# Kernel tuning notes

Measured on AMD Instinct MI355X. Metric: run time of the kernel, lower is better.

## Reference

```python
import jax, jax.numpy as jnp
import numpy as np

HIDDEN = 256


def setup_inputs() -> dict:
    key = jax.random.key(0)
    ks = jax.random.split(key, 6)
    b, c_len, q_len, h = 32, 1024, 128, HIDDEN
    # Xavier-uniform bounds for the learned weights
    lim_vec = float(np.sqrt(6.0 / (h + 1)))      # (h, 1) weights
    lim_cq = float(np.sqrt(6.0 / (1 + h)))       # (1, 1, h) weight
    return {
        "context": jax.random.normal(ks[0], (b, c_len, h), dtype=jnp.float32),
        "query": jax.random.normal(ks[1], (b, q_len, h), dtype=jnp.float32),
        "c_mask": jnp.zeros((b, c_len), dtype=bool),
        "q_mask": jnp.zeros((b, q_len), dtype=bool),
        "c_weight": jax.random.uniform(ks[2], (h, 1), jnp.float32, -lim_vec, lim_vec),
        "q_weight": jax.random.uniform(ks[3], (h, 1), jnp.float32, -lim_vec, lim_vec),
        "cq_weight": jax.random.uniform(ks[4], (1, 1, h), jnp.float32, -lim_cq, lim_cq),
        "bias": jnp.zeros((1,), dtype=jnp.float32),
    }


def reference(context, query, c_mask, q_mask, c_weight, q_weight, cq_weight, bias):
    # Trilinear similarity: S[b,i,j] = c_i.w_c + q_j.w_q + (c_i * w_cq).q_j + bias
    s0 = context @ c_weight                                  # (b, c, 1)
    s1 = jnp.swapaxes(query @ q_weight, 1, 2)                # (b, 1, q)
    s2 = jnp.einsum('bch,bqh->bcq', context * cq_weight, query)
    S = s0 + s1 + s2 + bias                                  # (b, c, q)

    S_bar = jax.nn.softmax(S, axis=1)       # softmax over context axis
    S_bar_bar = jax.nn.softmax(S, axis=2)   # softmax over query axis

    A = jnp.einsum('bcq,bqh->bch', S, query)  # note: raw S, as in source
    B = jnp.einsum('bcq,bkq,bkh->bch', S_bar, S_bar_bar, context)

    return jnp.concatenate([context, A, context * A, context * B], axis=2)
```

## Files before the change

### kernel.cpp

```cpp
#include <hip/hip_runtime.h>
#include <cstdint>
#include <cstddef>

#define BATCH 32
#define CLEN  1024
#define QLEN  128
#define HID   256

typedef __attribute__((ext_vector_type(8))) short bf16x8;
typedef __attribute__((ext_vector_type(4))) float f32x4;

#define MFMA(a, b, c) __builtin_amdgcn_mfma_f32_16x16x32_bf16((a), (b), (c), 0, 0, 0)

__device__ __forceinline__ ushort f2b(float f) {
    union { float f; uint u; } v; v.f = f;
    uint r = (v.u + 0x7fffu + ((v.u >> 16) & 1u)) >> 16;
    return (ushort)r;
}
__device__ __forceinline__ float b2f(ushort u) {
    union { uint u; float f; } v; v.u = ((uint)u) << 16;
    return v.f;
}

__global__ __launch_bounds__(256) void prep_kernel(
    const float* __restrict__ context, const float* __restrict__ query,
    const float* __restrict__ cw, const float* __restrict__ qw,
    const float* __restrict__ cqw,
    ushort* __restrict__ ctxT, ushort* __restrict__ mcB,
    ushort* __restrict__ qB, ushort* __restrict__ qT,
    float* __restrict__ cdot, float* __restrict__ qdot)
{
    __shared__ ushort lds[64][258];
    int bid = blockIdx.x;
    int t = threadIdx.x;
    int r = t >> 2, qd = t & 3;
    if (bid < 512) {
        int b = bid >> 4, c0 = (bid & 15) * 64;
        const float* src = context + ((size_t)(b * CLEN + c0 + r)) * HID;
        ushort* mcr = mcB + ((size_t)(b * CLEN + c0 + r)) * HID;
        float dot = 0.f;
        #pragma unroll
        for (int j = 0; j < 16; j++) {
            int h = j * 16 + qd * 4;
            float4 v  = *reinterpret_cast<const float4*>(src + h);
            float4 w  = *reinterpret_cast<const float4*>(cw + h);
            float4 wc = *reinterpret_cast<const float4*>(cqw + h);
            dot += v.x * w.x + v.y * w.y + v.z * w.z + v.w * w.w;
            uint p0 = (uint)f2b(v.x) | ((uint)f2b(v.y) << 16);
            uint p1 = (uint)f2b(v.z) | ((uint)f2b(v.w) << 16);
            *reinterpret_cast<uint*>(&lds[r][h])     = p0;
            *reinterpret_cast<uint*>(&lds[r][h + 2]) = p1;
            uint2 mc;
            mc.x = (uint)f2b(v.x * wc.x) | ((uint)f2b(v.y * wc.y) << 16);
            mc.y = (uint)f2b(v.z * wc.z) | ((uint)f2b(v.w * wc.w) << 16);
            *reinterpret_cast<uint2*>(mcr + h) = mc;
        }
        dot += __shfl_xor(dot, 1);
        dot += __shfl_xor(dot, 2);
        if (qd == 0) cdot[b * CLEN + c0 + r] = dot;
        __syncthreads();
        ushort* dst = ctxT + ((size_t)(b * HID + t)) * CLEN + c0;
        #pragma unroll
        for (int j = 0; j < 8; j++) {
            uint4 w;
            w.x = (uint)lds[j*8+0][t] | ((uint)lds[j*8+1][t] << 16);
            w.y = (uint)lds[j*8+2][t] | ((uint)lds[j*8+3][t] << 16);
            w.z = (uint)lds[j*8+4][t] | ((uint)lds[j*8+5][t] << 16);
            w.w = (uint)lds[j*8+6][t] | ((uint)lds[j*8+7][t] << 16);
            *reinterpret_cast<uint4*>(dst + j * 8) = w;
        }
    } else {
        int bb = bid - 512;
        int b = bb >> 1, q0 = (bb & 1) * 64;
        const float* src = query + ((size_t)(b * QLEN + q0 + r)) * HID;
        ushort* qBr = qB + ((size_t)(b * QLEN + q0 + r)) * HID;
        float dot = 0.f;
        #pragma unroll
        for (int j = 0; j < 16; j++) {
            int h = j * 16 + qd * 4;
            float4 v = *reinterpret_cast<const float4*>(src + h);
            float4 w = *reinterpret_cast<const float4*>(qw + h);
            dot += v.x * w.x + v.y * w.y + v.z * w.z + v.w * w.w;
            uint p0 = (uint)f2b(v.x) | ((uint)f2b(v.y) << 16);
            uint p1 = (uint)f2b(v.z) | ((uint)f2b(v.w) << 16);
            *reinterpret_cast<uint*>(&lds[r][h])     = p0;
            *reinterpret_cast<uint*>(&lds[r][h + 2]) = p1;
            uint2 pk; pk.x = p0; pk.y = p1;
            *reinterpret_cast<uint2*>(qBr + h) = pk;
        }
        dot += __shfl_xor(dot, 1);
        dot += __shfl_xor(dot, 2);
        if (qd == 0) qdot[b * QLEN + q0 + r] = dot;
        __syncthreads();
        ushort* dst = qT + ((size_t)(b * HID + t)) * QLEN + q0;
        #pragma unroll
        for (int j = 0; j < 8; j++) {
            uint4 w;
            w.x = (uint)lds[j*8+0][t] | ((uint)lds[j*8+1][t] << 16);
            w.y = (uint)lds[j*8+2][t] | ((uint)lds[j*8+3][t] << 16);
            w.z = (uint)lds[j*8+4][t] | ((uint)lds[j*8+5][t] << 16);
            w.w = (uint)lds[j*8+6][t] | ((uint)lds[j*8+7][t] << 16);
            *reinterpret_cast<uint4*>(dst + j * 8) = w;
        }
    }
}

__global__ __launch_bounds__(256) void s_kernel(
    const ushort* __restrict__ mcB, const ushort* __restrict__ qB,
    const float* __restrict__ cdot, const float* __restrict__ qdot,
    const float* __restrict__ bias,
    ushort* __restrict__ S, ushort* __restrict__ P2T)
{
    __shared__ float ldsS[64][132];
    __shared__ float ldsM[64], ldsR[64];
    int ct = blockIdx.x, b = blockIdx.y;
    int c0 = ct * 64;
    int t = threadIdx.x;
    int w = t >> 6, L = t & 63, g = L >> 4, ln = L & 15;
    int wr = w >> 1, wc = w & 1;

    f32x4 acc[2][4];
    #pragma unroll
    for (int mi = 0; mi < 2; mi++)
        #pragma unroll
        for (int ni = 0; ni < 4; ni++) acc[mi][ni] = (f32x4){0.f, 0.f, 0.f, 0.f};

    const ushort* aBase = mcB + ((size_t)(b * CLEN + c0 + wr * 32)) * HID;
    const ushort* qBb   = qB + ((size_t)(b * QLEN + wc * 64)) * HID;

    #pragma unroll 2
    for (int kk = 0; kk < 8; kk++) {
        int k = kk * 32 + g * 8;
        bf16x8 a[2], bq[4];
        #pragma unroll
        for (int mi = 0; mi < 2; mi++)
            a[mi] = *reinterpret_cast<const bf16x8*>(aBase + (size_t)(mi * 16 + ln) * HID + k);
        #pragma unroll
        for (int ni = 0; ni < 4; ni++)
            bq[ni] = *reinterpret_cast<const bf16x8*>(qBb + (size_t)(ni * 16 + ln) * HID + k);
        #pragma unroll
        for (int mi = 0; mi < 2; mi++)
            #pragma unroll
            for (int ni = 0; ni < 4; ni++)
                acc[mi][ni] = MFMA(a[mi], bq[ni], acc[mi][ni]);
    }

    float bv = bias[0];
    float qdv[4];
    #pragma unroll
    for (int ni = 0; ni < 4; ni++) qdv[ni] = qdot[b * QLEN + wc * 64 + ni * 16 + ln];
    #pragma unroll
    for (int mi = 0; mi < 2; mi++)
        #pragma unroll
        for (int r = 0; r < 4; r++) {
            int row = wr * 32 + mi * 16 + g * 4 + r;
            float cd = cdot[b * CLEN + c0 + row] + bv;
            #pragma unroll
            for (int ni = 0; ni < 4; ni++)
                ldsS[row][wc * 64 + ni * 16 + ln] = acc[mi][ni][r] + cd + qdv[ni];
        }
    __syncthreads();
    {
        int row = t >> 2, qs = (t & 3) * 32;
        float4 vr[8];
        float m = -1e30f;
        #pragma unroll
        for (int j = 0; j < 8; j++) {
            vr[j] = *reinterpret_cast<const float4*>(&ldsS[row][qs + j * 4]);
            m = fmaxf(m, fmaxf(fmaxf(vr[j].x, vr[j].y), fmaxf(vr[j].z, vr[j].w)));
        }
        m = fmaxf(m, __shfl_xor(m, 1));
        m = fmaxf(m, __shfl_xor(m, 2));
        float s = 0.f;
        #pragma unroll
        for (int j = 0; j < 8; j++)
            s += __expf(vr[j].x - m) + __expf(vr[j].y - m) +
                 __expf(vr[j].z - m) + __expf(vr[j].w - m);
        s += __shfl_xor(s, 1);
        s += __shfl_xor(s, 2);
        if ((t & 3) == 0) { ldsM[row] = m; ldsR[row] = 1.0f / s; }
    }
    __syncthreads();
    {
        const size_t Sbase = ((size_t)b * CLEN + c0) * QLEN;
        #pragma unroll
        for (int i = 0; i < 8; i++) {
            int flat = t + 256 * i;
            int q4 = flat & 31, c = flat >> 5;
            float4 v = *reinterpret_cast<const float4*>(&ldsS[c][q4 * 4]);
            uint2 pk;
            pk.x = (uint)f2b(v.x) | ((uint)f2b(v.y) << 16);
            pk.y = (uint)f2b(v.z) | ((uint)f2b(v.w) << 16);
            *reinterpret_cast<uint2*>(&S[Sbase + (size_t)c * QLEN + q4 * 4]) = pk;
        }
    }
    {
        int q = t >> 1, half = t & 1;
        ushort* dst = P2T + ((size_t)b * QLEN + q) * CLEN + c0 + half * 32;
        #pragma unroll
        for (int jo = 0; jo < 4; jo++) {
            uint pk[4];
            #pragma unroll
            for (int l = 0; l < 4; l++) {
                int c0l = half * 32 + jo * 8 + l * 2;
                float p0 = __expf(ldsS[c0l][q]     - ldsM[c0l])     * ldsR[c0l];
                float p1 = __expf(ldsS[c0l + 1][q] - ldsM[c0l + 1]) * ldsR[c0l + 1];
                pk[l] = (uint)f2b(p0) | ((uint)f2b(p1) << 16);
            }
            uint4 wv; wv.x = pk[0]; wv.y = pk[1]; wv.z = pk[2]; wv.w = pk[3];
            *reinterpret_cast<uint4*>(dst + jo * 8) = wv;
        }
    }
}

__global__ __launch_bounds__(256) void t_kernel(
    const ushort* __restrict__ ctxT, const ushort* __restrict__ P2T,
    float* __restrict__ Tpart)
{
    int x = blockIdx.x, b = blockIdx.y;
    int h0 = (x >> 1) * 64, ks = x & 1;
    int t = threadIdx.x;
    int w = t >> 6, L = t & 63, g = L >> 4, ln = L & 15;
    int wr = w >> 1, wc = w & 1;

    f32x4 acc[2][4];
    #pragma unroll
    for (int mi = 0; mi < 2; mi++)
        #pragma unroll
        for (int ni = 0; ni < 4; ni++) acc[mi][ni] = (f32x4){0.f, 0.f, 0.f, 0.f};

    const ushort* aB = ctxT + ((size_t)(b * HID + h0 + wr * 32)) * CLEN + ks * 512;
    const ushort* bB = P2T + ((size_t)(b * QLEN + wc * 64)) * CLEN + ks * 512;

    #pragma unroll 2
    for (int kk = 0; kk < 16; kk++) {
        int k = kk * 32 + g * 8;
        bf16x8 a[2], bq[4];
        #pragma unroll
        for (int mi = 0; mi < 2; mi++)
            a[mi] = *reinterpret_cast<const bf16x8*>(aB + (size_t)(mi * 16 + ln) * CLEN + k);
        #pragma unroll
        for (int ni = 0; ni < 4; ni++)
            bq[ni] = *reinterpret_cast<const bf16x8*>(bB + (size_t)(ni * 16 + ln) * CLEN + k);
        #pragma unroll
        for (int mi = 0; mi < 2; mi++)
            #pragma unroll
            for (int ni = 0; ni < 4; ni++)
                acc[mi][ni] = MFMA(a[mi], bq[ni], acc[mi][ni]);
    }
    float* dst = Tpart + (size_t)ks * (BATCH * HID * QLEN);
    #pragma unroll
    for (int mi = 0; mi < 2; mi++)
        #pragma unroll
        for (int ni = 0; ni < 4; ni++)
            #pragma unroll
            for (int r = 0; r < 4; r++) {
                int h = h0 + wr * 32 + mi * 16 + g * 4 + r;
                int q = wc * 64 + ni * 16 + ln;
                dst[((size_t)b * HID + h) * QLEN + q] = acc[mi][ni][r];
            }
}

__global__ __launch_bounds__(256) void ct_kernel(
    const ushort* __restrict__ S, const float* __restrict__ Tpart,
    ushort* __restrict__ Tt, float* __restrict__ colmax)
{
    __shared__ float red[4][2][8];
    __shared__ float MS[16], SR[16];
    int qc = blockIdx.x, b = blockIdx.y;
    int q0 = qc * 16;
    int t = threadIdx.x;
    int qh = t & 1, cg = t >> 1;
    int w = t >> 6, L = t & 63;
    const ushort* base = S + (size_t)b * CLEN * QLEN + q0 + qh * 8;
    float vm[8];
    #pragma unroll
    for (int j = 0; j < 8; j++) vm[j] = -1e30f;
    #pragma unroll
    for (int i = 0; i < 8; i++) {
        bf16x8 v = *reinterpret_cast<const bf16x8*>(base + (size_t)(cg + 128 * i) * QLEN);
        #pragma unroll
        for (int j = 0; j < 8; j++) vm[j] = fmaxf(vm[j], b2f((ushort)v[j]));
    }
    #pragma unroll
    for (int off = 2; off <= 32; off <<= 1)
        #pragma unroll
        for (int j = 0; j < 8; j++) vm[j] = fmaxf(vm[j], __shfl_xor(vm[j], off, 64));
    if (L < 2) {
        #pragma unroll
        for (int j = 0; j < 8; j++) red[w][L][j] = vm[j];
    }
    __syncthreads();
    if (t < 16) {
        int j = t & 7, qq = t >> 3;
        float m = fmaxf(fmaxf(red[0][qq][j], red[1][qq][j]),
                        fmaxf(red[2][qq][j], red[3][qq][j]));
        MS[qq * 8 + j] = m;
        colmax[b * QLEN + q0 + qq * 8 + j] = m;
    }
    __syncthreads();
    float M[8], sum[8];
    #pragma unroll
    for (int j = 0; j < 8; j++) { M[j] = MS[qh * 8 + j]; sum[j] = 0.f; }
    #pragma unroll
    for (int i = 0; i < 8; i++) {
        bf16x8 v = *reinterpret_cast<const bf16x8*>(base + (size_t)(cg + 128 * i) * QLEN);
        #pragma unroll
        for (int j = 0; j < 8; j++) sum[j] += __expf(b2f((ushort)v[j]) - M[j]);
    }
    #pragma unroll
    for (int off = 2; off <= 32; off <<= 1)
        #pragma unroll
        for (int j = 0; j < 8; j++) sum[j] += __shfl_xor(sum[j], off, 64);
    __syncthreads();
    if (L < 2) {
        #pragma unroll
        for (int j = 0; j < 8; j++) red[w][L][j] = sum[j];
    }
    __syncthreads();
    if (t < 16) {
        int j = t & 7, qq = t >> 3;
        float s = red[0][qq][j] + red[1][qq][j] + red[2][qq][j] + red[3][qq][j];
        SR[qq * 8 + j] = 1.0f / s;
    }
    __syncthreads();
    const float* p0 = Tpart + ((size_t)b * HID + t) * QLEN + q0;
    const float* p1 = p0 + (size_t)BATCH * HID * QLEN;
    uint pk[8];
    #pragma unroll
    for (int seg = 0; seg < 4; seg++) {
        float4 xa = *reinterpret_cast<const float4*>(p0 + seg * 4);
        float4 xb = *reinterpret_cast<const float4*>(p1 + seg * 4);
        float r0 = (xa.x + xb.x) * SR[seg * 4 + 0];
        float r1 = (xa.y + xb.y) * SR[seg * 4 + 1];
        float r2 = (xa.z + xb.z) * SR[seg * 4 + 2];
        float r3 = (xa.w + xb.w) * SR[seg * 4 + 3];
        pk[seg * 2 + 0] = (uint)f2b(r0) | ((uint)f2b(r1) << 16);
        pk[seg * 2 + 1] = (uint)f2b(r2) | ((uint)f2b(r3) << 16);
    }
    ushort* dst = Tt + ((size_t)b * HID + t) * QLEN + q0;
    uint4 w0; w0.x = pk[0]; w0.y = pk[1]; w0.z = pk[2]; w0.w = pk[3];
    uint4 w1; w1.x = pk[4]; w1.y = pk[5]; w1.z = pk[6]; w1.w = pk[7];
    *reinterpret_cast<uint4*>(dst)     = w0;
    *reinterpret_cast<uint4*>(dst + 8) = w1;
}

__global__ __launch_bounds__(256) void ab_out_kernel(
    const ushort* __restrict__ S, const ushort* __restrict__ qT,
    const ushort* __restrict__ Tt, const float* __restrict__ context,
    const float* __restrict__ colmax, float* __restrict__ out)
{
    __shared__ float ldsA[64][68];
    __shared__ float ldsB[64][68];
    int x = blockIdx.x, b = blockIdx.y;
    int c0 = (x >> 1) * 64, h0 = (x & 1) * 128;
    int t = threadIdx.x;
    int wc = t >> 6, L = t & 63, g = L >> 4, ln = L & 15;

    f32x4 accA[4][2], accB[4][2];
    #pragma unroll
    for (int mi = 0; mi < 4; mi++)
        #pragma unroll
        for (int ni = 0; ni < 2; ni++) {
            accA[mi][ni] = (f32x4){0.f, 0.f, 0.f, 0.f};
            accB[mi][ni] = (f32x4){0.f, 0.f, 0.f, 0.f};
        }

    const ushort* Srow = S + ((size_t)(b * CLEN + c0)) * QLEN;
    const ushort* qTb  = qT + ((size_t)(b * HID + h0 + wc * 32)) * QLEN;
    const ushort* TtB  = Tt + ((size_t)(b * HID + h0 + wc * 32)) * QLEN;
    const float* cmB = colmax + b * QLEN;

    #pragma unroll
    for (int kk = 0; kk < 4; kk++) {
        int k = kk * 32 + g * 8;
        float4 cm0 = *reinterpret_cast<const float4*>(cmB + k);
        float4 cm1 = *reinterpret_cast<const float4*>(cmB + k + 4);
        float cmv[8] = {cm0.x, cm0.y, cm0.z, cm0.w, cm1.x, cm1.y, cm1.z, cm1.w};
        bf16x8 sa[4], pa[4], bq[2], bt[2];
        #pragma unroll
        for (int mi = 0; mi < 4; mi++) {
            sa[mi] = *reinterpret_cast<const bf16x8*>(Srow + (size_t)(mi * 16 + ln) * QLEN + k);
            bf16x8 pv;
            #pragma unroll
            for (int i = 0; i < 8; i++)
                pv[i] = (short)f2b(__expf(b2f((ushort)sa[mi][i]) - cmv[i]));
            pa[mi] = pv;
        }
        #pragma unroll
        for (int ni = 0; ni < 2; ni++) {
            bq[ni] = *reinterpret_cast<const bf16x8*>(qTb + (size_t)(ni * 16 + ln) * QLEN + k);
            bt[ni] = *reinterpret_cast<const bf16x8*>(TtB + (size_t)(ni * 16 + ln) * QLEN + k);
        }
        #pragma unroll
        for (int mi = 0; mi < 4; mi++)
            #pragma unroll
            for (int ni = 0; ni < 2; ni++) {
                accA[mi][ni] = MFMA(sa[mi], bq[ni], accA[mi][ni]);
                accB[mi][ni] = MFMA(pa[mi], bt[ni], accB[mi][ni]);
            }
    }

    #pragma unroll
    for (int hh = 0; hh < 2; hh++) {
        if ((wc >> 1) == hh) {
            int hc = wc & 1;
            #pragma unroll
            for (int mi = 0; mi < 4; mi++)
                #pragma unroll
                for (int ni = 0; ni < 2; ni++)
                    #pragma unroll
                    for (int r = 0; r < 4; r++) {
                        ldsA[mi * 16 + g * 4 + r][hc * 32 + ni * 16 + ln] = accA[mi][ni][r];
                        ldsB[mi * 16 + g * 4 + r][hc * 32 + ni * 16 + ln] = accB[mi][ni][r];
                    }
        }
        __syncthreads();
        #pragma unroll
        for (int i = 0; i < 4; i++) {
            int flat = t + 256 * i;
            int h4 = flat & 15, c = flat >> 4;
            float4 av = *reinterpret_cast<const float4*>(&ldsA[c][h4 * 4]);
            float4 bv = *reinterpret_cast<const float4*>(&ldsB[c][h4 * 4]);
            float4 cv = *reinterpret_cast<const float4*>(
                context + ((size_t)(b * CLEN + c0 + c)) * HID + h0 + hh * 64 + h4 * 4);
            size_t o = ((size_t)(b * CLEN + c0 + c)) * 1024 + h0 + hh * 64 + h4 * 4;
            *reinterpret_cast<float4*>(&out[o])       = cv;
            *reinterpret_cast<float4*>(&out[o + 256]) = av;
            *reinterpret_cast<float4*>(&out[o + 512]) =
                make_float4(cv.x * av.x, cv.y * av.y, cv.z * av.z, cv.w * av.w);
            *reinterpret_cast<float4*>(&out[o + 768]) =
                make_float4(cv.x * bv.x, cv.y * bv.y, cv.z * bv.z, cv.w * bv.w);
        }
        __syncthreads();
    }
}

extern "C" void kernel_launch(void* const* d_in, const int* in_sizes, int n_in,
                              void* d_out, int out_size, void* d_ws, size_t ws_size,
                              hipStream_t stream)
{
    (void)in_sizes; (void)n_in; (void)out_size; (void)ws_size;
    const float* context   = (const float*)d_in[0];
    const float* query     = (const float*)d_in[1];
    const float* c_weight  = (const float*)d_in[4];
    const float* q_weight  = (const float*)d_in[5];
    const float* cq_weight = (const float*)d_in[6];
    const float* bias      = (const float*)d_in[7];
    float* out = (float*)d_out;
    char* wsb  = (char*)d_ws;

    ushort* ctxT = (ushort*)(wsb);
    ushort* mcB  = (ushort*)(wsb + 16777216);
    ushort* qB   = (ushort*)(wsb + 33554432);
    ushort* qT   = (ushort*)(wsb + 35651584);
    ushort* S    = (ushort*)(wsb + 37748736);
    ushort* P2T  = (ushort*)(wsb + 46137344);
    ushort* Tt   = (ushort*)(wsb + 54525952);
    float*  Tpart = (float*)(wsb + 56623104);
    float*  cdot  = (float*)(wsb + 65011712);
    float*  qdot   = cdot + 32768;
    float*  colmax = qdot + 4096;

    prep_kernel<<<576, 256, 0, stream>>>(context, query, c_weight, q_weight,
                                         cq_weight, ctxT, mcB, qB, qT, cdot, qdot);
    s_kernel<<<dim3(16, 32), 256, 0, stream>>>(mcB, qB, cdot, qdot, bias, S, P2T);
    t_kernel<<<dim3(8, 32), 256, 0, stream>>>(ctxT, P2T, Tpart);
    ct_kernel<<<dim3(8, 32), 256, 0, stream>>>(S, Tpart, Tt, colmax);
    ab_out_kernel<<<dim3(32, 32), 256, 0, stream>>>(S, qT, Tt, context, colmax, out);
}
```

Measured before the change: 106.4 us.

## Fuse column softmax sums into S kernel and drop separate column-reduction kernel

Moves the cq_weight scaling from the context side to the query side and stores a plain bf16 copy of context. The S kernel now computes per-tile column sums of exp(S) and uses a last-block atomic counter to produce reciprocal column sums. The dedicated column max/sum kernel and the split-K fp32 Tpart buffer are removed; t_kernel instead runs full-K with the normalisation applied in its epilogue. The final kernel reads bf16 context rather than fp32, cutting memory traffic. In exchange, the column softmax no longer subtracts the max, so large S values can overflow, and the passthrough context columns of the output lose precision to bf16.

```diff
diff --git a/kernel.cpp b/kernel.cpp
--- a/kernel.cpp
+++ b/kernel.cpp
@@ -26,34 +26,33 @@
     const float* __restrict__ context, const float* __restrict__ query,
     const float* __restrict__ cw, const float* __restrict__ qw,
     const float* __restrict__ cqw,
-    ushort* __restrict__ ctxT, ushort* __restrict__ mcB,
-    ushort* __restrict__ qB, ushort* __restrict__ qT,
-    float* __restrict__ cdot, float* __restrict__ qdot)
+    ushort* __restrict__ ctxB, ushort* __restrict__ ctxT,
+    ushort* __restrict__ qmB, ushort* __restrict__ qT,
+    float* __restrict__ cdot, float* __restrict__ qdot,
+    int* __restrict__ counter)
 {
     __shared__ ushort lds[64][258];
     int bid = blockIdx.x;
     int t = threadIdx.x;
+    if (bid == 0 && t < BATCH) counter[t] = 0;
     int r = t >> 2, qd = t & 3;
     if (bid < 512) {
         int b = bid >> 4, c0 = (bid & 15) * 64;
         const float* src = context + ((size_t)(b * CLEN + c0 + r)) * HID;
-        ushort* mcr = mcB + ((size_t)(b * CLEN + c0 + r)) * HID;
+        ushort* cbr = ctxB + ((size_t)(b * CLEN + c0 + r)) * HID;
         float dot = 0.f;
         #pragma unroll
         for (int j = 0; j < 16; j++) {
             int h = j * 16 + qd * 4;
-            float4 v  = *reinterpret_cast<const float4*>(src + h);
-            float4 w  = *reinterpret_cast<const float4*>(cw + h);
-            float4 wc = *reinterpret_cast<const float4*>(cqw + h);
+            float4 v = *reinterpret_cast<const float4*>(src + h);
+            float4 w = *reinterpret_cast<const float4*>(cw + h);
             dot += v.x * w.x + v.y * w.y + v.z * w.z + v.w * w.w;
             uint p0 = (uint)f2b(v.x) | ((uint)f2b(v.y) << 16);
             uint p1 = (uint)f2b(v.z) | ((uint)f2b(v.w) << 16);
             *reinterpret_cast<uint*>(&lds[r][h])     = p0;
             *reinterpret_cast<uint*>(&lds[r][h + 2]) = p1;
-            uint2 mc;
-            mc.x = (uint)f2b(v.x * wc.x) | ((uint)f2b(v.y * wc.y) << 16);
-            mc.y = (uint)f2b(v.z * wc.z) | ((uint)f2b(v.w * wc.w) << 16);
-            *reinterpret_cast<uint2*>(mcr + h) = mc;
+            uint2 pk; pk.x = p0; pk.y = p1;
+            *reinterpret_cast<uint2*>(cbr + h) = pk;
         }
         dot += __shfl_xor(dot, 1);
         dot += __shfl_xor(dot, 2);
@@ -73,20 +72,23 @@
         int bb = bid - 512;
         int b = bb >> 1, q0 = (bb & 1) * 64;
         const float* src = query + ((size_t)(b * QLEN + q0 + r)) * HID;
-        ushort* qBr = qB + ((size_t)(b * QLEN + q0 + r)) * HID;
+        ushort* qmr = qmB + ((size_t)(b * QLEN + q0 + r)) * HID;
         float dot = 0.f;
         #pragma unroll
         for (int j = 0; j < 16; j++) {
             int h = j * 16 + qd * 4;
-            float4 v = *reinterpret_cast<const float4*>(src + h);
-            float4 w = *reinterpret_cast<const float4*>(qw + h);
+            float4 v   = *reinterpret_cast<const float4*>(src + h);
+            float4 w   = *reinterpret_cast<const float4*>(qw + h);
+            float4 wc4 = *reinterpret_cast<const float4*>(cqw + h);
             dot += v.x * w.x + v.y * w.y + v.z * w.z + v.w * w.w;
             uint p0 = (uint)f2b(v.x) | ((uint)f2b(v.y) << 16);
             uint p1 = (uint)f2b(v.z) | ((uint)f2b(v.w) << 16);
             *reinterpret_cast<uint*>(&lds[r][h])     = p0;
             *reinterpret_cast<uint*>(&lds[r][h + 2]) = p1;
-            uint2 pk; pk.x = p0; pk.y = p1;
-            *reinterpret_cast<uint2*>(qBr + h) = pk;
+            uint2 mc;
+            mc.x = (uint)f2b(v.x * wc4.x) | ((uint)f2b(v.y * wc4.y) << 16);
+            mc.y = (uint)f2b(v.z * wc4.z) | ((uint)f2b(v.w * wc4.w) << 16);
+            *reinterpret_cast<uint2*>(qmr + h) = mc;
         }
         dot += __shfl_xor(dot, 1);
         dot += __shfl_xor(dot, 2);
@@ -106,13 +108,16 @@
 }
 
 __global__ __launch_bounds__(256) void s_kernel(
-    const ushort* __restrict__ mcB, const ushort* __restrict__ qB,
+    const ushort* __restrict__ ctxB, const ushort* __restrict__ qmB,
     const float* __restrict__ cdot, const float* __restrict__ qdot,
     const float* __restrict__ bias,
-    ushort* __restrict__ S, ushort* __restrict__ P2T)
+    ushort* __restrict__ S, ushort* __restrict__ P2T,
+    float* __restrict__ psum, float* __restrict__ colsumr,
+    int* __restrict__ counter)
 {
     __shared__ float ldsS[64][132];
     __shared__ float ldsM[64], ldsR[64];
+    __shared__ int lastFlag;
     int ct = blockIdx.x, b = blockIdx.y;
     int c0 = ct * 64;
     int t = threadIdx.x;
@@ -125,8 +130,8 @@
         #pragma unroll
         for (int ni = 0; ni < 4; ni++) acc[mi][ni] = (f32x4){0.f, 0.f, 0.f, 0.f};
 
-    const ushort* aBase = mcB + ((size_t)(b * CLEN + c0 + wr * 32)) * HID;
-    const ushort* qBb   = qB + ((size_t)(b * QLEN + wc * 64)) * HID;
+    const ushort* aBase = ctxB + ((size_t)(b * CLEN + c0 + wr * 32)) * HID;
+    const ushort* qBb   = qmB + ((size_t)(b * QLEN + wc * 64)) * HID;
 
     #pragma unroll 2
     for (int kk = 0; kk < 8; kk++) {
@@ -211,151 +216,83 @@
             *reinterpret_cast<uint4*>(dst + jo * 8) = wv;
         }
     }
+    {
+        int q = t >> 1, half = t & 1;
+        float s = 0.f;
+        #pragma unroll
+        for (int cc = 0; cc < 32; cc++)
+            s += __expf(b2f(f2b(ldsS[half * 32 + cc][q])));
+        s += __shfl_xor(s, 1);
+        if (half == 0) psum[((size_t)b * 16 + ct) * QLEN + q] = s;
+    }
+    __syncthreads();
+    if (t == 0) {
+        __threadfence();
+        int v = atomicAdd(&counter[b], 1);
+        lastFlag = (v == 15);
+    }
+    __syncthreads();
+    if (lastFlag) {
+        __threadfence();
+        if (t < QLEN) {
+            float s = 0.f;
+            #pragma unroll
+            for (int j = 0; j < 16; j++)
+                s += psum[((size_t)b * 16 + j) * QLEN + t];
+            colsumr[b * QLEN + t] = 1.0f / s;
+        }
+    }
 }
 
 __global__ __launch_bounds__(256) void t_kernel(
     const ushort* __restrict__ ctxT, const ushort* __restrict__ P2T,
-    float* __restrict__ Tpart)
+    const float* __restrict__ colsumr, ushort* __restrict__ Tt)
 {
     int x = blockIdx.x, b = blockIdx.y;
-    int h0 = (x >> 1) * 64, ks = x & 1;
+    int h0 = (x >> 1) * 32, q0 = (x & 1) * 64;
     int t = threadIdx.x;
     int w = t >> 6, L = t & 63, g = L >> 4, ln = L & 15;
     int wr = w >> 1, wc = w & 1;
 
-    f32x4 acc[2][4];
-    #pragma unroll
-    for (int mi = 0; mi < 2; mi++)
-        #pragma unroll
-        for (int ni = 0; ni < 4; ni++) acc[mi][ni] = (f32x4){0.f, 0.f, 0.f, 0.f};
-
-    const ushort* aB = ctxT + ((size_t)(b * HID + h0 + wr * 32)) * CLEN + ks * 512;
-    const ushort* bB = P2T + ((size_t)(b * QLEN + wc * 64)) * CLEN + ks * 512;
-
-    #pragma unroll 2
-    for (int kk = 0; kk < 16; kk++) {
+    f32x4 acc[2];
+    acc[0] = (f32x4){0.f, 0.f, 0.f, 0.f};
+    acc[1] = (f32x4){0.f, 0.f, 0.f, 0.f};
+
+    const ushort* aB = ctxT + ((size_t)(b * HID + h0 + wr * 16)) * CLEN;
+    const ushort* bB = P2T + ((size_t)(b * QLEN + q0 + wc * 32)) * CLEN;
+
+    #pragma unroll 4
+    for (int kk = 0; kk < 32; kk++) {
         int k = kk * 32 + g * 8;
-        bf16x8 a[2], bq[4];
-        #pragma unroll
-        for (int mi = 0; mi < 2; mi++)
-            a[mi] = *reinterpret_cast<const bf16x8*>(aB + (size_t)(mi * 16 + ln) * CLEN + k);
-        #pragma unroll
-        for (int ni = 0; ni < 4; ni++)
-            bq[ni] = *reinterpret_cast<const bf16x8*>(bB + (size_t)(ni * 16 + ln) * CLEN + k);
-        #pragma unroll
-        for (int mi = 0; mi < 2; mi++)
-            #pragma unroll
-            for (int ni = 0; ni < 4; ni++)
-                acc[mi][ni] = MFMA(a[mi], bq[ni], acc[mi][ni]);
-    }
-    float* dst = Tpart + (size_t)ks * (BATCH * HID * QLEN);
-    #pragma unroll
-    for (int mi = 0; mi < 2; mi++)
-        #pragma unroll
-        for (int ni = 0; ni < 4; ni++)
-            #pragma unroll
-            for (int r = 0; r < 4; r++) {
-                int h = h0 + wr * 32 + mi * 16 + g * 4 + r;
-                int q = wc * 64 + ni * 16 + ln;
-                dst[((size_t)b * HID + h) * QLEN + q] = acc[mi][ni][r];
-            }
-}
-
-__global__ __launch_bounds__(256) void ct_kernel(
-    const ushort* __restrict__ S, const float* __restrict__ Tpart,
-    ushort* __restrict__ Tt, float* __restrict__ colmax)
-{
-    __shared__ float red[4][2][8];
-    __shared__ float MS[16], SR[16];
-    int qc = blockIdx.x, b = blockIdx.y;
-    int q0 = qc * 16;
-    int t = threadIdx.x;
-    int qh = t & 1, cg = t >> 1;
-    int w = t >> 6, L = t & 63;
-    const ushort* base = S + (size_t)b * CLEN * QLEN + q0 + qh * 8;
-    float vm[8];
-    #pragma unroll
-    for (int j = 0; j < 8; j++) vm[j] = -1e30f;
-    #pragma unroll
-    for (int i = 0; i < 8; i++) {
-        bf16x8 v = *reinterpret_cast<const bf16x8*>(base + (size_t)(cg + 128 * i) * QLEN);
-        #pragma unroll
-        for (int j = 0; j < 8; j++) vm[j] = fmaxf(vm[j], b2f((ushort)v[j]));
-    }
-    #pragma unroll
-    for (int off = 2; off <= 32; off <<= 1)
-        #pragma unroll
-        for (int j = 0; j < 8; j++) vm[j] = fmaxf(vm[j], __shfl_xor(vm[j], off, 64));
-    if (L < 2) {
-        #pragma unroll
-        for (int j = 0; j < 8; j++) red[w][L][j] = vm[j];
-    }
-    __syncthreads();
-    if (t < 16) {
-        int j = t & 7, qq = t >> 3;
-        float m = fmaxf(fmaxf(red[0][qq][j], red[1][qq][j]),
-                        fmaxf(red[2][qq][j], red[3][qq][j]));
-        MS[qq * 8 + j] = m;
-        colmax[b * QLEN + q0 + qq * 8 + j] = m;
-    }
-    __syncthreads();
-    float M[8], sum[8];
-    #pragma unroll
-    for (int j = 0; j < 8; j++) { M[j] = MS[qh * 8 + j]; sum[j] = 0.f; }
-    #pragma unroll
-    for (int i = 0; i < 8; i++) {
-        bf16x8 v = *reinterpret_cast<const bf16x8*>(base + (size_t)(cg + 128 * i) * QLEN);
-        #pragma unroll
-        for (int j = 0; j < 8; j++) sum[j] += __expf(b2f((ushort)v[j]) - M[j]);
-    }
-    #pragma unroll
-    for (int off = 2; off <= 32; off <<= 1)
-        #pragma unroll
-        for (int j = 0; j < 8; j++) sum[j] += __shfl_xor(sum[j], off, 64);
-    __syncthreads();
-    if (L < 2) {
-        #pragma unroll
-        for (int j = 0; j < 8; j++) red[w][L][j] = sum[j];
-    }
-    __syncthreads();
-    if (t < 16) {
-        int j = t & 7, qq = t >> 3;
-        float s = red[0][qq][j] + red[1][qq][j] + red[2][qq][j] + red[3][qq][j];
-        SR[qq * 8 + j] = 1.0f / s;
-    }
-    __syncthreads();
-    const float* p0 = Tpart + ((size_t)b * HID + t) * QLEN + q0;
-    const float* p1 = p0 + (size_t)BATCH * HID * QLEN;
-    uint pk[8];
-    #pragma unroll
-    for (int seg = 0; seg < 4; seg++) {
-        float4 xa = *reinterpret_cast<const float4*>(p0 + seg * 4);
-        float4 xb = *reinterpret_cast<const float4*>(p1 + seg * 4);
-        float r0 = (xa.x + xb.x) * SR[seg * 4 + 0];
-        float r1 = (xa.y + xb.y) * SR[seg * 4 + 1];
-        float r2 = (xa.z + xb.z) * SR[seg * 4 + 2];
-        float r3 = (xa.w + xb.w) * SR[seg * 4 + 3];
-        pk[seg * 2 + 0] = (uint)f2b(r0) | ((uint)f2b(r1) << 16);
-        pk[seg * 2 + 1] = (uint)f2b(r2) | ((uint)f2b(r3) << 16);
-    }
-    ushort* dst = Tt + ((size_t)b * HID + t) * QLEN + q0;
-    uint4 w0; w0.x = pk[0]; w0.y = pk[1]; w0.z = pk[2]; w0.w = pk[3];
-    uint4 w1; w1.x = pk[4]; w1.y = pk[5]; w1.z = pk[6]; w1.w = pk[7];
-    *reinterpret_cast<uint4*>(dst)     = w0;
-    *reinterpret_cast<uint4*>(dst + 8) = w1;
+        bf16x8 a  = *reinterpret_cast<const bf16x8*>(aB + (size_t)ln * CLEN + k);
+        bf16x8 b0 = *reinterpret_cast<const bf16x8*>(bB + (size_t)ln * CLEN + k);
+        bf16x8 b1 = *reinterpret_cast<const bf16x8*>(bB + (size_t)(16 + ln) * CLEN + k);
+        acc[0] = MFMA(a, b0, acc[0]);
+        acc[1] = MFMA(a, b1, acc[1]);
+    }
+    #pragma unroll
+    for (int ni = 0; ni < 2; ni++) {
+        int q = q0 + wc * 32 + ni * 16 + ln;
+        float cr = colsumr[b * QLEN + q];
+        #pragma unroll
+        for (int r = 0; r < 4; r++) {
+            int h = h0 + wr * 16 + g * 4 + r;
+            Tt[((size_t)b * HID + h) * QLEN + q] = f2b(acc[ni][r] * cr);
+        }
+    }
 }
 
 __global__ __launch_bounds__(256) void ab_out_kernel(
     const ushort* __restrict__ S, const ushort* __restrict__ qT,
-    const ushort* __restrict__ Tt, const float* __restrict__ context,
-    const float* __restrict__ colmax, float* __restrict__ out)
+    const ushort* __restrict__ Tt, const ushort* __restrict__ ctxB,
+    float* __restrict__ out)
 {
     __shared__ float ldsA[64][68];
     __shared__ float ldsB[64][68];
     int x = blockIdx.x, b = blockIdx.y;
     int c0 = (x >> 1) * 64, h0 = (x & 1) * 128;
     int t = threadIdx.x;
-    int wc = t >> 6, L = t & 63, g = L >> 4, ln = L & 15;
+    int wv = t >> 6, L = t & 63, g = L >> 4, ln = L & 15;
 
     f32x4 accA[4][2], accB[4][2];
     #pragma unroll
@@ -367,16 +304,12 @@
         }
 
     const ushort* Srow = S + ((size_t)(b * CLEN + c0)) * QLEN;
-    const ushort* qTb  = qT + ((size_t)(b * HID + h0 + wc * 32)) * QLEN;
-    const ushort* TtB  = Tt + ((size_t)(b * HID + h0 + wc * 32)) * QLEN;
-    const float* cmB = colmax + b * QLEN;
+    const ushort* qTb  = qT + ((size_t)(b * HID + h0 + wv * 32)) * QLEN;
+    const ushort* TtB  = Tt + ((size_t)(b * HID + h0 + wv * 32)) * QLEN;
 
     #pragma unroll
     for (int kk = 0; kk < 4; kk++) {
         int k = kk * 32 + g * 8;
-        float4 cm0 = *reinterpret_cast<const float4*>(cmB + k);
-        float4 cm1 = *reinterpret_cast<const float4*>(cmB + k + 4);
-        float cmv[8] = {cm0.x, cm0.y, cm0.z, cm0.w, cm1.x, cm1.y, cm1.z, cm1.w};
         bf16x8 sa[4], pa[4], bq[2], bt[2];
         #pragma unroll
         for (int mi = 0; mi < 4; mi++) {
@@ -384,7 +317,7 @@
             bf16x8 pv;
             #pragma unroll
             for (int i = 0; i < 8; i++)
-                pv[i] = (short)f2b(__expf(b2f((ushort)sa[mi][i]) - cmv[i]));
+                pv[i] = (short)f2b(__expf(b2f((ushort)sa[mi][i])));
             pa[mi] = pv;
         }
         #pragma unroll
@@ -403,8 +336,8 @@
 
     #pragma unroll
     for (int hh = 0; hh < 2; hh++) {
-        if ((wc >> 1) == hh) {
-            int hc = wc & 1;
+        if ((wv >> 1) == hh) {
+            int hc = wv & 1;
             #pragma unroll
             for (int mi = 0; mi < 4; mi++)
                 #pragma unroll
@@ -417,20 +350,31 @@
         }
         __syncthreads();
         #pragma unroll
-        for (int i = 0; i < 4; i++) {
+        for (int i = 0; i < 2; i++) {
             int flat = t + 256 * i;
-            int h4 = flat & 15, c = flat >> 4;
-            float4 av = *reinterpret_cast<const float4*>(&ldsA[c][h4 * 4]);
-            float4 bv = *reinterpret_cast<const float4*>(&ldsB[c][h4 * 4]);
-            float4 cv = *reinterpret_cast<const float4*>(
-                context + ((size_t)(b * CLEN + c0 + c)) * HID + h0 + hh * 64 + h4 * 4);
-            size_t o = ((size_t)(b * CLEN + c0 + c)) * 1024 + h0 + hh * 64 + h4 * 4;
-            *reinterpret_cast<float4*>(&out[o])       = cv;
-            *reinterpret_cast<float4*>(&out[o + 256]) = av;
+            int h8 = flat & 7, c = flat >> 3;
+            bf16x8 cb = *reinterpret_cast<const bf16x8*>(
+                ctxB + ((size_t)(b * CLEN + c0 + c)) * HID + h0 + hh * 64 + h8 * 8);
+            float cf[8];
+            #pragma unroll
+            for (int j = 0; j < 8; j++) cf[j] = b2f((ushort)cb[j]);
+            float4 a0 = *reinterpret_cast<const float4*>(&ldsA[c][h8 * 8]);
+            float4 a1 = *reinterpret_cast<const float4*>(&ldsA[c][h8 * 8 + 4]);
+            float4 b0 = *reinterpret_cast<const float4*>(&ldsB[c][h8 * 8]);
+            float4 b1 = *reinterpret_cast<const float4*>(&ldsB[c][h8 * 8 + 4]);
+            size_t o = ((size_t)(b * CLEN + c0 + c)) * 1024 + h0 + hh * 64 + h8 * 8;
+            *reinterpret_cast<float4*>(&out[o])     = make_float4(cf[0], cf[1], cf[2], cf[3]);
+            *reinterpret_cast<float4*>(&out[o + 4]) = make_float4(cf[4], cf[5], cf[6], cf[7]);
+            *reinterpret_cast<float4*>(&out[o + 256]) = a0;
+            *reinterpret_cast<float4*>(&out[o + 260]) = a1;
             *reinterpret_cast<float4*>(&out[o + 512]) =
-                make_float4(cv.x * av.x, cv.y * av.y, cv.z * av.z, cv.w * av.w);
+                make_float4(cf[0] * a0.x, cf[1] * a0.y, cf[2] * a0.z, cf[3] * a0.w);
+            *reinterpret_cast<float4*>(&out[o + 516]) =
+                make_float4(cf[4] * a1.x, cf[5] * a1.y, cf[6] * a1.z, cf[7] * a1.w);
             *reinterpret_cast<float4*>(&out[o + 768]) =
-                make_float4(cv.x * bv.x, cv.y * bv.y, cv.z * bv.z, cv.w * bv.w);
+                make_float4(cf[0] * b0.x, cf[1] * b0.y, cf[2] * b0.z, cf[3] * b0.w);
+            *reinterpret_cast<float4*>(&out[o + 772]) =
+                make_float4(cf[4] * b1.x, cf[5] * b1.y, cf[6] * b1.z, cf[7] * b1.w);
         }
         __syncthreads();
     }
@@ -450,22 +394,24 @@
     float* out = (float*)d_out;
     char* wsb  = (char*)d_ws;
 
-    ushort* ctxT = (ushort*)(wsb);
-    ushort* mcB  = (ushort*)(wsb + 16777216);
-    ushort* qB   = (ushort*)(wsb + 33554432);
+    ushort* ctxB = (ushort*)(wsb);
+    ushort* ctxT = (ushort*)(wsb + 16777216);
+    ushort* qmB  = (ushort*)(wsb + 33554432);
     ushort* qT   = (ushort*)(wsb + 35651584);
     ushort* S    = (ushort*)(wsb + 37748736);
     ushort* P2T  = (ushort*)(wsb + 46137344);
     ushort* Tt   = (ushort*)(wsb + 54525952);
-    float*  Tpart = (float*)(wsb + 56623104);
-    float*  cdot  = (float*)(wsb + 65011712);
-    float*  qdot   = cdot + 32768;
-    float*  colmax = qdot + 4096;
+    float*  cdot    = (float*)(wsb + 56623104);
+    float*  qdot    = cdot + 32768;
+    float*  colsumr = qdot + 4096;
+    float*  psum    = colsumr + 4096;
+    int*    counter = (int*)(psum + 65536);
 
     prep_kernel<<<576, 256, 0, stream>>>(context, query, c_weight, q_weight,
-                                         cq_weight, ctxT, mcB, qB, qT, cdot, qdot);
-    s_kernel<<<dim3(16, 32), 256, 0, stream>>>(mcB, qB, cdot, qdot, bias, S, P2T);
-    t_kernel<<<dim3(8, 32), 256, 0, stream>>>(ctxT, P2T, Tpart);
-    ct_kernel<<<dim3(8, 32), 256, 0, stream>>>(S, Tpart, Tt, colmax);
-    ab_out_kernel<<<dim3(32, 32), 256, 0, stream>>>(S, qT, Tt, context, colmax, out);
-}
+                                         cq_weight, ctxB, ctxT, qmB, qT,
+                                         cdot, qdot, counter);
+    s_kernel<<<dim3(16, 32), 256, 0, stream>>>(ctxB, qmB, cdot, qdot, bias,
+                                               S, P2T, psum, colsumr, counter);
+    t_kernel<<<dim3(16, 32), 256, 0, stream>>>(ctxT, P2T, colsumr, Tt);
+    ab_out_kernel<<<dim3(32, 32), 256, 0, stream>>>(S, qT, Tt, ctxB, out);
+}
```

New measurement: 131.1 us. 23.3% more time.
